# Performance work log

Hardware: AMD Instinct MI355X
Metric: run time of the kernel (lower is better)

Reference implementation:

```python
import jax, jax.numpy as jnp
import numpy as np

B, C, H, W = 8, 256, 128, 128
QK = 64

def setup_inputs() -> dict:
    key = jax.random.key(0)
    ks = jax.random.split(key, 8)
    s = 0.02
    return {
        "x": jax.random.normal(ks[0], (B, C, H, W), dtype=jnp.float32),
        "wq": jax.random.normal(ks[1], (QK, C), dtype=jnp.float32) * s,
        "bq": jax.random.normal(ks[2], (QK,), dtype=jnp.float32) * s,
        "wk": jax.random.normal(ks[3], (QK, C), dtype=jnp.float32) * s,
        "bk": jax.random.normal(ks[4], (QK,), dtype=jnp.float32) * s,
        "wv": jax.random.normal(ks[5], (C, C), dtype=jnp.float32) * s,
        "bv": jax.random.normal(ks[6], (C,), dtype=jnp.float32) * s,
        "gamma": jax.random.normal(ks[7], (1,), dtype=jnp.float32) * 0.1,
    }

def reference(x, wq, bq, wk, bk, wv, bv, gamma):
    # 1x1 convs == per-pixel linear projections over channels
    Q = jnp.einsum('bchw,oc->bohw', x, wq) + bq[None, :, None, None]  # (b,qk,h,w)
    K = jnp.einsum('bchw,oc->bohw', x, wk) + bk[None, :, None, None]  # (b,qk,h,w)
    V = jnp.einsum('bchw,oc->bohw', x, wv) + bv[None, :, None, None]  # (b,c,h,w)
    # row attention: for each (b,h) row, scores over width pairs
    scores = jnp.einsum('bchw,bchv->bhwv', Q, K)          # (b,h,w_q,w_k)
    attn = jax.nn.softmax(scores, axis=-1)                # softmax over keys (dim=2 after bmm)
    out = jnp.einsum('bchv,bhwv->bchw', V, attn)          # (b,c,h,w)
    return gamma[0] * out + x
```

## Files before the change

kernel.cpp:

```cpp
#include <hip/hip_runtime.h>
#include <hip/hip_bf16.h>


typedef short bf16x8 __attribute__((ext_vector_type(8)));
typedef float f32x4 __attribute__((ext_vector_type(4)));
using u32 = unsigned int;
using u16 = unsigned short;

#define XT_OFF   0
#define XT_SB    528
#define SA_OFF   67584
#define SB_OFF   85056
#define QT_OFF   67584
#define KT_OFF   86016
#define QK_SB    144
#define PL_OFF   67584
#define PL_SB    272
#define WP_OFF   104448
#define VL_OFF   141312
#define VL_SB    272
#define BIAS_OFF 158720
#define LDS_TOTAL 160256

#define WS_WQK   0
#define WS_WV    73728

__device__ __forceinline__ u16 bfbits(float f) {
    __hip_bfloat16 h = __float2bfloat16(f);
    u16 u; __builtin_memcpy(&u, &h, 2); return u;
}
__device__ __forceinline__ u32 packbf2(float a, float b) {
    return (u32)bfbits(a) | ((u32)bfbits(b) << 16);
}
__device__ __forceinline__ float bf2f(u16 u) {
    union { u32 i; float f; } v; v.i = ((u32)u) << 16; return v.f;
}

__device__ __forceinline__ void gl2lds16(const char* g, const char* l) {
    __builtin_amdgcn_global_load_lds(
        (const __attribute__((address_space(1))) void*)(unsigned long long)g,
        (__attribute__((address_space(3))) void*)(u32)(unsigned long long)l,
        16, 0, 0);
}
__device__ __forceinline__ void stage18k(const char* g, const char* lds, int w, int l) {
    gl2lds16(g + w * 1024 + l * 16,        lds + w * 1024);
    gl2lds16(g + 8192 + w * 1024 + l * 16, lds + 8192 + w * 1024);
    if (l < 16) gl2lds16(g + 16384 + w * 256 + l * 16, lds + 16384 + w * 256);
}
__device__ __forceinline__ void stage36k(const char* g, const char* lds, int w, int l) {
#pragma unroll
    for (int r = 0; r < 4; ++r)
        gl2lds16(g + r * 8192 + w * 1024 + l * 16, lds + r * 8192 + w * 1024);
    if (l < 32) gl2lds16(g + 32768 + w * 512 + l * 16, lds + 32768 + w * 512);
}

__device__ __forceinline__ void hard_barrier() {
    __builtin_amdgcn_sched_barrier(0);
    asm volatile("s_barrier" ::: "memory");
    __builtin_amdgcn_sched_barrier(0);
}

__global__ void prep_weights(const float* __restrict__ wq, const float* __restrict__ wk,
                             const float* __restrict__ wv, u32* __restrict__ ws) {
    int i = blockIdx.x * 256 + threadIdx.x;
    if (i >= 55296) return;
    u32 v = 0;
    if (i < 18432) {
        int c = i / 2304, rem = i % 2304;
        int row = rem / 36, iw = rem % 36;
        int kc = c >> 1;
        const float* m = (c & 1) ? wk : wq;
        if (iw < 32) {
            int col = kc * 64 + iw * 2;
            v = packbf2(m[row * 256 + col], m[row * 256 + col + 1]);
        }
    } else {
        int j = i - 18432;
        int c = j / 2304, rem = j % 2304;
        int row = rem / 36, iw = rem % 36;
        int mc = c >> 2, kc = c & 3;
        if (iw < 32) {
            int col = kc * 64 + iw * 2;
            v = packbf2(wv[(mc * 64 + row) * 256 + col], wv[(mc * 64 + row) * 256 + col + 1]);
        }
    }
    ws[i] = v;
}

__global__ __launch_bounds__(512, 1) void rowattn_mfma(
    const float* __restrict__ x,
    const float* __restrict__ bq,
    const float* __restrict__ bk,
    const float* __restrict__ bv,
    const float* __restrict__ gamma,
    const char* __restrict__ wsp,
    float* __restrict__ out)
{
    __shared__ __align__(16) char smem[LDS_TOTAL];
    const int t  = threadIdx.x;
    const int bh = blockIdx.x;
    const int b  = bh >> 7;
    const int h  = bh & 127;
    const int l  = t & 63;
    const int a  = l & 15;
    const int q  = l >> 4;
    const int nw = __builtin_amdgcn_readfirstlane(t >> 6);

    const char* wqk_g = wsp + WS_WQK;
    const char* wv_g  = wsp + WS_WV;
    const float g = gamma[0];

    stage18k(wqk_g,         smem + WP_OFF,         nw, l);
    stage18k(wqk_g + 18432, smem + WP_OFF + 18432, nw, l);

    float* biasl = (float*)(smem + BIAS_OFF);
    if (t < 384) {
        float v;
        if (t < 64) v = bq[t];
        else if (t < 128) v = bk[t - 64];
        else v = bv[t - 128];
        biasl[t] = v;
    }

    const int cl = t >> 5;
    const int w4 = (t & 31) * 4;
    const float* xb = x + ((b * 256 + cl) * 128 + h) * 128 + w4;
    float4 xr[16];
#pragma unroll
    for (int p = 0; p < 8; ++p) {
        xr[2 * p]     = *(const float4*)(xb + (p * 32) * 16384);
        xr[2 * p + 1] = *(const float4*)(xb + (p * 32 + 16) * 16384);
    }

    const int wrd = t >> 2;
    const int c8  = (t & 3) * 8;
#define SCW(c, w) ((c) * 136 + ((c) >> 3) * 8 + (w))
    {
        float* s0 = (float*)(smem + SA_OFF);
        *(float4*)&s0[SCW(cl, w4)]      = xr[0];
        *(float4*)&s0[SCW(cl + 16, w4)] = xr[1];
    }
    __syncthreads();
#pragma unroll
    for (int p = 0; p < 8; ++p) {
        float* sp = (float*)(smem + ((p & 1) ? SB_OFF : SA_OFF));
        if (p < 7) {
            float* sn = (float*)(smem + ((p & 1) ? SA_OFF : SB_OFF));
            *(float4*)&sn[SCW(cl, w4)]      = xr[2 * p + 2];
            *(float4*)&sn[SCW(cl + 16, w4)] = xr[2 * p + 3];
        }
        const float* sr = sp + SCW(c8, wrd);
        float s0 = sr[0],       s1 = sr[136],     s2 = sr[2 * 136], s3 = sr[3 * 136];
        float s4 = sr[4 * 136], s5 = sr[5 * 136], s6 = sr[6 * 136], s7 = sr[7 * 136];
        uint4 pk;
        pk.x = packbf2(s0, s1); pk.y = packbf2(s2, s3);
        pk.z = packbf2(s4, s5); pk.w = packbf2(s6, s7);
        *(uint4*)(smem + XT_OFF + wrd * XT_SB + (p * 32 + c8) * 2) = pk;
        __syncthreads();
    }
#undef SCW

    {
        f32x4 accQ[4], accK[4];
#pragma unroll
        for (int mt = 0; mt < 4; ++mt) {
            f32x4 cq, ck;
#pragma unroll
            for (int r = 0; r < 4; ++r) {
                cq[r] = biasl[mt * 16 + q * 4 + r];
                ck[r] = biasl[64 + mt * 16 + q * 4 + r];
            }
            accQ[mt] = cq; accK[mt] = ck;
        }
#pragma unroll
        for (int kc = 0; kc < 4; ++kc) {
            if (kc == 2) {
                asm volatile("s_waitcnt vmcnt(3)" ::: "memory");
                hard_barrier();
            }
            if (kc == 3) __syncthreads();
            const char* wqp = smem + WP_OFF + (kc & 1) * 18432;
            const char* wkp = wqp + 9216;
#pragma unroll
            for (int ks = 0; ks < 2; ++ks) {
                bf16x8 bx = *(const bf16x8*)(smem + XT_OFF + (nw * 16 + a) * XT_SB + (kc * 64 + ks * 32) * 2 + q * 16);
#pragma unroll
                for (int mt = 0; mt < 4; ++mt) {
                    bf16x8 aq = *(const bf16x8*)(wqp + (mt * 16 + a) * 144 + ks * 64 + q * 16);
                    accQ[mt] = __builtin_amdgcn_mfma_f32_16x16x32_bf16(aq, bx, accQ[mt], 0, 0, 0);
                    bf16x8 ak = *(const bf16x8*)(wkp + (mt * 16 + a) * 144 + ks * 64 + q * 16);
                    accK[mt] = __builtin_amdgcn_mfma_f32_16x16x32_bf16(ak, bx, accK[mt], 0, 0, 0);
                }
            }
            if (kc == 0) { __syncthreads(); stage18k(wqk_g + 2 * 18432, smem + WP_OFF,         nw, l); }
            if (kc == 1) { __syncthreads(); stage18k(wqk_g + 3 * 18432, smem + WP_OFF + 18432, nw, l); }
        }
#pragma unroll
        for (int mt = 0; mt < 4; ++mt) {
            uint2 pq; pq.x = packbf2(accQ[mt][0], accQ[mt][1]); pq.y = packbf2(accQ[mt][2], accQ[mt][3]);
            *(uint2*)(smem + QT_OFF + (nw * 16 + a) * QK_SB + (mt * 16 + q * 4) * 2) = pq;
            uint2 pk; pk.x = packbf2(accK[mt][0], accK[mt][1]); pk.y = packbf2(accK[mt][2], accK[mt][3]);
            *(uint2*)(smem + KT_OFF + (nw * 16 + a) * QK_SB + (mt * 16 + q * 4) * 2) = pk;
        }
    }
    __syncthreads();

    stage36k(wv_g, smem + WP_OFF, nw, l);
    f32x4 st[8];
#pragma unroll
    for (int mt = 0; mt < 8; ++mt) st[mt] = (f32x4){0.f, 0.f, 0.f, 0.f};
#pragma unroll
    for (int ks = 0; ks < 2; ++ks) {
        bf16x8 bqf = *(const bf16x8*)(smem + QT_OFF + (nw * 16 + a) * QK_SB + ks * 64 + q * 16);
#pragma unroll
        for (int mt = 0; mt < 8; ++mt) {
            bf16x8 akf = *(const bf16x8*)(smem + KT_OFF + (mt * 16 + a) * QK_SB + ks * 64 + q * 16);
            st[mt] = __builtin_amdgcn_mfma_f32_16x16x32_bf16(akf, bqf, st[mt], 0, 0, 0);
        }
    }
    {
        float mx = -3.0e38f;
#pragma unroll
        for (int mt = 0; mt < 8; ++mt)
#pragma unroll
            for (int r = 0; r < 4; ++r) mx = fmaxf(mx, st[mt][r]);
        mx = fmaxf(mx, __shfl_xor(mx, 16, 64));
        mx = fmaxf(mx, __shfl_xor(mx, 32, 64));
        float sum = 0.f;
#pragma unroll
        for (int mt = 0; mt < 8; ++mt)
#pragma unroll
            for (int r = 0; r < 4; ++r) { float e = __expf(st[mt][r] - mx); st[mt][r] = e; sum += e; }
        sum += __shfl_xor(sum, 16, 64);
        sum += __shfl_xor(sum, 32, 64);
        float inv = 1.0f / sum;
        hard_barrier();
#pragma unroll
        for (int mt = 0; mt < 8; ++mt) {
            uint2 pp; pp.x = packbf2(st[mt][0] * inv, st[mt][1] * inv);
            pp.y = packbf2(st[mt][2] * inv, st[mt][3] * inv);
            *(uint2*)(smem + PL_OFF + (nw * 16 + a) * PL_SB + (mt * 16 + q * 4) * 2) = pp;
        }
    }

#pragma unroll 1
    for (int mc = 0; mc < 4; ++mc) {
        __syncthreads();
        f32x4 accV[4];
#pragma unroll
        for (int mt = 0; mt < 4; ++mt) {
            f32x4 cv;
#pragma unroll
            for (int r = 0; r < 4; ++r) cv[r] = biasl[128 + mc * 64 + mt * 16 + q * 4 + r];
            accV[mt] = cv;
        }
#pragma unroll
        for (int kc = 0; kc < 4; ++kc) {
            const char* wvp = smem + WP_OFF + kc * 9216;
#pragma unroll
            for (int ks = 0; ks < 2; ++ks) {
                bf16x8 bx = *(const bf16x8*)(smem + XT_OFF + (nw * 16 + a) * XT_SB + (kc * 64 + ks * 32) * 2 + q * 16);
#pragma unroll
                for (int mt = 0; mt < 4; ++mt) {
                    bf16x8 av = *(const bf16x8*)(wvp + (mt * 16 + a) * 144 + ks * 64 + q * 16);
                    accV[mt] = __builtin_amdgcn_mfma_f32_16x16x32_bf16(av, bx, accV[mt], 0, 0, 0);
                }
            }
        }
#pragma unroll
        for (int mt = 0; mt < 4; ++mt)
#pragma unroll
            for (int r = 0; r < 4; ++r)
                *(u16*)(smem + VL_OFF + (mt * 16 + q * 4 + r) * VL_SB + (nw * 16 + a) * 2) = bfbits(accV[mt][r]);
        __syncthreads();
        if (mc < 3) stage36k(wv_g + (mc + 1) * 36864, smem + WP_OFF, nw, l);
        f32x4 accO[4];
#pragma unroll
        for (int mt = 0; mt < 4; ++mt) accO[mt] = (f32x4){0.f, 0.f, 0.f, 0.f};
#pragma unroll
        for (int ks = 0; ks < 4; ++ks) {
            bf16x8 bp = *(const bf16x8*)(smem + PL_OFF + (nw * 16 + a) * PL_SB + ks * 64 + q * 16);
#pragma unroll
            for (int mt = 0; mt < 4; ++mt) {
                bf16x8 av = *(const bf16x8*)(smem + VL_OFF + (mt * 16 + a) * VL_SB + ks * 64 + q * 16);
                accO[mt] = __builtin_amdgcn_mfma_f32_16x16x32_bf16(av, bp, accO[mt], 0, 0, 0);
            }
        }
#pragma unroll
        for (int mt = 0; mt < 4; ++mt) {
#pragma unroll
            for (int r = 0; r < 4; ++r) {
                int c = mc * 64 + mt * 16 + q * 4 + r;
                int w = nw * 16 + a;
                u16 xv = *(const u16*)(smem + XT_OFF + w * XT_SB + c * 2);
                out[((b * 256 + c) * 128 + h) * 128 + w] = g * accO[mt][r] + bf2f(xv);
            }
        }
    }
}

extern "C" void kernel_launch(void* const* d_in, const int* in_sizes, int n_in,
                              void* d_out, int out_size, void* d_ws, size_t ws_size,
                              hipStream_t stream) {
    const float* x     = (const float*)d_in[0];
    const float* wq    = (const float*)d_in[1];
    const float* bq    = (const float*)d_in[2];
    const float* wk    = (const float*)d_in[3];
    const float* bk    = (const float*)d_in[4];
    const float* wv    = (const float*)d_in[5];
    const float* bv    = (const float*)d_in[6];
    const float* gamma = (const float*)d_in[7];
    float* out = (float*)d_out;

    hipLaunchKernelGGL(prep_weights, dim3(216), dim3(256), 0, stream, wq, wk, wv, (u32*)d_ws);
    hipLaunchKernelGGL(rowattn_mfma, dim3(1024), dim3(512), 0, stream,
                       x, bq, bk, bv, gamma, (const char*)d_ws, out);
}
```

Before: 338.4 us.

## Double workgroup to 16 waves with 2D wave tiling and split-softmax merge

Raises the block from 8 to 16 waves and tiles each GEMM stage over a 4x4 wave grid (output-row tile by 32-wide pixel tile) instead of giving each wave a 16-pixel strip. Softmax across keys is now split over four waves, with per-wave max and sum merged through LDS. The aim is more waves to hide latency and fewer registers per thread (fewer x loads held, smaller accumulators). The cost is extra barriers and an LDS reduction step for the softmax. Operand reuse per wave also drops, so more LDS fragment loads are issued per MFMA.

```diff
diff --git a/kernel.cpp b/kernel.cpp
--- a/kernel.cpp
+++ b/kernel.cpp
@@ -19,6 +19,7 @@
 #define WP_OFF   104448
 #define VL_OFF   141312
 #define VL_SB    272
+#define SMP_OFF  141312
 #define BIAS_OFF 158720
 #define LDS_TOTAL 160256
 
@@ -43,20 +44,23 @@
         16, 0, 0);
 }
 __device__ __forceinline__ void stage18k(const char* g, const char* lds, int w, int l) {
-    gl2lds16(g + w * 1024 + l * 16,        lds + w * 1024);
-    gl2lds16(g + 8192 + w * 1024 + l * 16, lds + 8192 + w * 1024);
-    if (l < 16) gl2lds16(g + 16384 + w * 256 + l * 16, lds + 16384 + w * 256);
+    gl2lds16(g + w * 1024 + l * 16, lds + w * 1024);
+    if (l < 8) gl2lds16(g + 16384 + w * 128 + l * 16, lds + 16384 + w * 128);
 }
 __device__ __forceinline__ void stage36k(const char* g, const char* lds, int w, int l) {
-#pragma unroll
-    for (int r = 0; r < 4; ++r)
-        gl2lds16(g + r * 8192 + w * 1024 + l * 16, lds + r * 8192 + w * 1024);
-    if (l < 32) gl2lds16(g + 32768 + w * 512 + l * 16, lds + 32768 + w * 512);
+    gl2lds16(g + w * 1024 + l * 16,         lds + w * 1024);
+    gl2lds16(g + 16384 + w * 1024 + l * 16, lds + 16384 + w * 1024);
+    if (l < 16) gl2lds16(g + 32768 + w * 256 + l * 16, lds + 32768 + w * 256);
 }
 
 __device__ __forceinline__ void hard_barrier() {
     __builtin_amdgcn_sched_barrier(0);
     asm volatile("s_barrier" ::: "memory");
+    __builtin_amdgcn_sched_barrier(0);
+}
+__device__ __forceinline__ void lgkm_barrier() {
+    __builtin_amdgcn_sched_barrier(0);
+    asm volatile("s_waitcnt lgkmcnt(0)\n\ts_barrier" ::: "memory");
     __builtin_amdgcn_sched_barrier(0);
 }
 
@@ -87,7 +91,7 @@
     ws[i] = v;
 }
 
-__global__ __launch_bounds__(512, 1) void rowattn_mfma(
+__global__ __launch_bounds__(1024, 1) void rowattn_mfma(
     const float* __restrict__ x,
     const float* __restrict__ bq,
     const float* __restrict__ bk,
@@ -104,14 +108,17 @@
     const int l  = t & 63;
     const int a  = l & 15;
     const int q  = l >> 4;
-    const int nw = __builtin_amdgcn_readfirstlane(t >> 6);
+    const int wid = __builtin_amdgcn_readfirstlane(t >> 6);
+    const int mi = wid >> 2;
+    const int nj = wid & 3;
+    const int w0 = nj * 32;
 
     const char* wqk_g = wsp + WS_WQK;
     const char* wv_g  = wsp + WS_WV;
     const float g = gamma[0];
 
-    stage18k(wqk_g,         smem + WP_OFF,         nw, l);
-    stage18k(wqk_g + 18432, smem + WP_OFF + 18432, nw, l);
+    stage18k(wqk_g,         smem + WP_OFF,         wid, l);
+    stage18k(wqk_g + 18432, smem + WP_OFF + 18432, wid, l);
 
     float* biasl = (float*)(smem + BIAS_OFF);
     if (t < 384) {
@@ -125,57 +132,50 @@
     const int cl = t >> 5;
     const int w4 = (t & 31) * 4;
     const float* xb = x + ((b * 256 + cl) * 128 + h) * 128 + w4;
-    float4 xr[16];
-#pragma unroll
-    for (int p = 0; p < 8; ++p) {
-        xr[2 * p]     = *(const float4*)(xb + (p * 32) * 16384);
-        xr[2 * p + 1] = *(const float4*)(xb + (p * 32 + 16) * 16384);
-    }
-
-    const int wrd = t >> 2;
-    const int c8  = (t & 3) * 8;
+    float4 xr[8];
+#pragma unroll
+    for (int p = 0; p < 8; ++p) xr[p] = *(const float4*)(xb + (p * 32) * 16384);
+
+    const int wrd = t >> 3;
+    const int c4  = (t & 7) * 4;
 #define SCW(c, w) ((c) * 136 + ((c) >> 3) * 8 + (w))
     {
         float* s0 = (float*)(smem + SA_OFF);
-        *(float4*)&s0[SCW(cl, w4)]      = xr[0];
-        *(float4*)&s0[SCW(cl + 16, w4)] = xr[1];
-    }
-    __syncthreads();
+        *(float4*)&s0[SCW(cl, w4)] = xr[0];
+    }
+    lgkm_barrier();
 #pragma unroll
     for (int p = 0; p < 8; ++p) {
         float* sp = (float*)(smem + ((p & 1) ? SB_OFF : SA_OFF));
         if (p < 7) {
             float* sn = (float*)(smem + ((p & 1) ? SA_OFF : SB_OFF));
-            *(float4*)&sn[SCW(cl, w4)]      = xr[2 * p + 2];
-            *(float4*)&sn[SCW(cl + 16, w4)] = xr[2 * p + 3];
-        }
-        const float* sr = sp + SCW(c8, wrd);
-        float s0 = sr[0],       s1 = sr[136],     s2 = sr[2 * 136], s3 = sr[3 * 136];
-        float s4 = sr[4 * 136], s5 = sr[5 * 136], s6 = sr[6 * 136], s7 = sr[7 * 136];
-        uint4 pk;
-        pk.x = packbf2(s0, s1); pk.y = packbf2(s2, s3);
-        pk.z = packbf2(s4, s5); pk.w = packbf2(s6, s7);
-        *(uint4*)(smem + XT_OFF + wrd * XT_SB + (p * 32 + c8) * 2) = pk;
-        __syncthreads();
+            *(float4*)&sn[SCW(cl, w4)] = xr[p + 1];
+        }
+        const float* sr = sp + SCW(c4, wrd);
+        float s0 = sr[0], s1 = sr[136], s2 = sr[2 * 136], s3 = sr[3 * 136];
+        uint2 pk; pk.x = packbf2(s0, s1); pk.y = packbf2(s2, s3);
+        *(uint2*)(smem + XT_OFF + wrd * XT_SB + (p * 32 + c4) * 2) = pk;
+        if (p < 7) lgkm_barrier();
     }
 #undef SCW
+    __syncthreads();
 
     {
-        f32x4 accQ[4], accK[4];
-#pragma unroll
-        for (int mt = 0; mt < 4; ++mt) {
+        f32x4 accQ[2], accK[2];
+#pragma unroll
+        for (int nt = 0; nt < 2; ++nt) {
             f32x4 cq, ck;
 #pragma unroll
             for (int r = 0; r < 4; ++r) {
-                cq[r] = biasl[mt * 16 + q * 4 + r];
-                ck[r] = biasl[64 + mt * 16 + q * 4 + r];
-            }
-            accQ[mt] = cq; accK[mt] = ck;
+                cq[r] = biasl[mi * 16 + q * 4 + r];
+                ck[r] = biasl[64 + mi * 16 + q * 4 + r];
+            }
+            accQ[nt] = cq; accK[nt] = ck;
         }
 #pragma unroll
         for (int kc = 0; kc < 4; ++kc) {
             if (kc == 2) {
-                asm volatile("s_waitcnt vmcnt(3)" ::: "memory");
+                asm volatile("s_waitcnt vmcnt(2)" ::: "memory");
                 hard_barrier();
             }
             if (kc == 3) __syncthreads();
@@ -183,117 +183,150 @@
             const char* wkp = wqp + 9216;
 #pragma unroll
             for (int ks = 0; ks < 2; ++ks) {
-                bf16x8 bx = *(const bf16x8*)(smem + XT_OFF + (nw * 16 + a) * XT_SB + (kc * 64 + ks * 32) * 2 + q * 16);
-#pragma unroll
-                for (int mt = 0; mt < 4; ++mt) {
-                    bf16x8 aq = *(const bf16x8*)(wqp + (mt * 16 + a) * 144 + ks * 64 + q * 16);
-                    accQ[mt] = __builtin_amdgcn_mfma_f32_16x16x32_bf16(aq, bx, accQ[mt], 0, 0, 0);
-                    bf16x8 ak = *(const bf16x8*)(wkp + (mt * 16 + a) * 144 + ks * 64 + q * 16);
-                    accK[mt] = __builtin_amdgcn_mfma_f32_16x16x32_bf16(ak, bx, accK[mt], 0, 0, 0);
+                bf16x8 aq = *(const bf16x8*)(wqp + (mi * 16 + a) * 144 + ks * 64 + q * 16);
+                bf16x8 ak = *(const bf16x8*)(wkp + (mi * 16 + a) * 144 + ks * 64 + q * 16);
+#pragma unroll
+                for (int nt = 0; nt < 2; ++nt) {
+                    bf16x8 bx = *(const bf16x8*)(smem + XT_OFF + (w0 + nt * 16 + a) * XT_SB + (kc * 64 + ks * 32) * 2 + q * 16);
+                    accQ[nt] = __builtin_amdgcn_mfma_f32_16x16x32_bf16(aq, bx, accQ[nt], 0, 0, 0);
+                    accK[nt] = __builtin_amdgcn_mfma_f32_16x16x32_bf16(ak, bx, accK[nt], 0, 0, 0);
                 }
             }
-            if (kc == 0) { __syncthreads(); stage18k(wqk_g + 2 * 18432, smem + WP_OFF,         nw, l); }
-            if (kc == 1) { __syncthreads(); stage18k(wqk_g + 3 * 18432, smem + WP_OFF + 18432, nw, l); }
-        }
-#pragma unroll
-        for (int mt = 0; mt < 4; ++mt) {
-            uint2 pq; pq.x = packbf2(accQ[mt][0], accQ[mt][1]); pq.y = packbf2(accQ[mt][2], accQ[mt][3]);
-            *(uint2*)(smem + QT_OFF + (nw * 16 + a) * QK_SB + (mt * 16 + q * 4) * 2) = pq;
-            uint2 pk; pk.x = packbf2(accK[mt][0], accK[mt][1]); pk.y = packbf2(accK[mt][2], accK[mt][3]);
-            *(uint2*)(smem + KT_OFF + (nw * 16 + a) * QK_SB + (mt * 16 + q * 4) * 2) = pk;
+            if (kc == 0) { hard_barrier(); stage18k(wqk_g + 2 * 18432, smem + WP_OFF,         wid, l); }
+            if (kc == 1) { hard_barrier(); stage18k(wqk_g + 3 * 18432, smem + WP_OFF + 18432, wid, l); }
+        }
+#pragma unroll
+        for (int nt = 0; nt < 2; ++nt) {
+            const int wrow = w0 + nt * 16 + a;
+            uint2 pq; pq.x = packbf2(accQ[nt][0], accQ[nt][1]); pq.y = packbf2(accQ[nt][2], accQ[nt][3]);
+            *(uint2*)(smem + QT_OFF + wrow * QK_SB + (mi * 16 + q * 4) * 2) = pq;
+            uint2 pk; pk.x = packbf2(accK[nt][0], accK[nt][1]); pk.y = packbf2(accK[nt][2], accK[nt][3]);
+            *(uint2*)(smem + KT_OFF + wrow * QK_SB + (mi * 16 + q * 4) * 2) = pk;
         }
     }
     __syncthreads();
 
-    stage36k(wv_g, smem + WP_OFF, nw, l);
-    f32x4 st[8];
-#pragma unroll
-    for (int mt = 0; mt < 8; ++mt) st[mt] = (f32x4){0.f, 0.f, 0.f, 0.f};
+    stage36k(wv_g, smem + WP_OFF, wid, l);
+    f32x4 st[2][2];
+#pragma unroll
+    for (int mt2 = 0; mt2 < 2; ++mt2)
+#pragma unroll
+        for (int nt = 0; nt < 2; ++nt) st[mt2][nt] = (f32x4){0.f, 0.f, 0.f, 0.f};
 #pragma unroll
     for (int ks = 0; ks < 2; ++ks) {
-        bf16x8 bqf = *(const bf16x8*)(smem + QT_OFF + (nw * 16 + a) * QK_SB + ks * 64 + q * 16);
-#pragma unroll
-        for (int mt = 0; mt < 8; ++mt) {
-            bf16x8 akf = *(const bf16x8*)(smem + KT_OFF + (mt * 16 + a) * QK_SB + ks * 64 + q * 16);
-            st[mt] = __builtin_amdgcn_mfma_f32_16x16x32_bf16(akf, bqf, st[mt], 0, 0, 0);
-        }
+        bf16x8 bq0 = *(const bf16x8*)(smem + QT_OFF + (w0 + a) * QK_SB + ks * 64 + q * 16);
+        bf16x8 bq1 = *(const bf16x8*)(smem + QT_OFF + (w0 + 16 + a) * QK_SB + ks * 64 + q * 16);
+        bf16x8 ak0 = *(const bf16x8*)(smem + KT_OFF + (mi * 32 + a) * QK_SB + ks * 64 + q * 16);
+        bf16x8 ak1 = *(const bf16x8*)(smem + KT_OFF + (mi * 32 + 16 + a) * QK_SB + ks * 64 + q * 16);
+        st[0][0] = __builtin_amdgcn_mfma_f32_16x16x32_bf16(ak0, bq0, st[0][0], 0, 0, 0);
+        st[0][1] = __builtin_amdgcn_mfma_f32_16x16x32_bf16(ak0, bq1, st[0][1], 0, 0, 0);
+        st[1][0] = __builtin_amdgcn_mfma_f32_16x16x32_bf16(ak1, bq0, st[1][0], 0, 0, 0);
+        st[1][1] = __builtin_amdgcn_mfma_f32_16x16x32_bf16(ak1, bq1, st[1][1], 0, 0, 0);
     }
     {
-        float mx = -3.0e38f;
-#pragma unroll
-        for (int mt = 0; mt < 8; ++mt)
-#pragma unroll
-            for (int r = 0; r < 4; ++r) mx = fmaxf(mx, st[mt][r]);
-        mx = fmaxf(mx, __shfl_xor(mx, 16, 64));
-        mx = fmaxf(mx, __shfl_xor(mx, 32, 64));
-        float sum = 0.f;
-#pragma unroll
-        for (int mt = 0; mt < 8; ++mt)
-#pragma unroll
-            for (int r = 0; r < 4; ++r) { float e = __expf(st[mt][r] - mx); st[mt][r] = e; sum += e; }
-        sum += __shfl_xor(sum, 16, 64);
-        sum += __shfl_xor(sum, 32, 64);
-        float inv = 1.0f / sum;
-        hard_barrier();
-#pragma unroll
-        for (int mt = 0; mt < 8; ++mt) {
-            uint2 pp; pp.x = packbf2(st[mt][0] * inv, st[mt][1] * inv);
-            pp.y = packbf2(st[mt][2] * inv, st[mt][3] * inv);
-            *(uint2*)(smem + PL_OFF + (nw * 16 + a) * PL_SB + (mt * 16 + q * 4) * 2) = pp;
+        float pmax[2], psum[2];
+#pragma unroll
+        for (int nt = 0; nt < 2; ++nt) {
+            float mx = -3.0e38f;
+#pragma unroll
+            for (int mt2 = 0; mt2 < 2; ++mt2)
+#pragma unroll
+                for (int r = 0; r < 4; ++r) mx = fmaxf(mx, st[mt2][nt][r]);
+            mx = fmaxf(mx, __shfl_xor(mx, 16, 64));
+            mx = fmaxf(mx, __shfl_xor(mx, 32, 64));
+            float s = 0.f;
+#pragma unroll
+            for (int mt2 = 0; mt2 < 2; ++mt2)
+#pragma unroll
+                for (int r = 0; r < 4; ++r) {
+                    float e = __expf(st[mt2][nt][r] - mx); st[mt2][nt][r] = e; s += e;
+                }
+            s += __shfl_xor(s, 16, 64);
+            s += __shfl_xor(s, 32, 64);
+            pmax[nt] = mx; psum[nt] = s;
+        }
+        float2* smp = (float2*)(smem + SMP_OFF);
+        if (q == 0) {
+#pragma unroll
+            for (int nt = 0; nt < 2; ++nt)
+                smp[(w0 + nt * 16 + a) * 4 + mi] = make_float2(pmax[nt], psum[nt]);
+        }
+        lgkm_barrier();
+        float f[2];
+#pragma unroll
+        for (int nt = 0; nt < 2; ++nt) {
+            const int wq = w0 + nt * 16 + a;
+            float2 p0 = smp[wq * 4 + 0], p1 = smp[wq * 4 + 1];
+            float2 p2 = smp[wq * 4 + 2], p3 = smp[wq * 4 + 3];
+            float m = fmaxf(fmaxf(p0.x, p1.x), fmaxf(p2.x, p3.x));
+            float s = p0.y * __expf(p0.x - m) + p1.y * __expf(p1.x - m)
+                    + p2.y * __expf(p2.x - m) + p3.y * __expf(p3.x - m);
+            f[nt] = __expf(pmax[nt] - m) / s;
+        }
+#pragma unroll
+        for (int nt = 0; nt < 2; ++nt) {
+            const int wq = w0 + nt * 16 + a;
+#pragma unroll
+            for (int mt2 = 0; mt2 < 2; ++mt2) {
+                uint2 pp;
+                pp.x = packbf2(st[mt2][nt][0] * f[nt], st[mt2][nt][1] * f[nt]);
+                pp.y = packbf2(st[mt2][nt][2] * f[nt], st[mt2][nt][3] * f[nt]);
+                *(uint2*)(smem + PL_OFF + wq * PL_SB + (mi * 32 + mt2 * 16 + q * 4) * 2) = pp;
+            }
         }
     }
 
 #pragma unroll 1
     for (int mc = 0; mc < 4; ++mc) {
         __syncthreads();
-        f32x4 accV[4];
-#pragma unroll
-        for (int mt = 0; mt < 4; ++mt) {
+        f32x4 accV[2];
+        {
             f32x4 cv;
 #pragma unroll
-            for (int r = 0; r < 4; ++r) cv[r] = biasl[128 + mc * 64 + mt * 16 + q * 4 + r];
-            accV[mt] = cv;
+            for (int r = 0; r < 4; ++r) cv[r] = biasl[128 + mc * 64 + mi * 16 + q * 4 + r];
+            accV[0] = cv; accV[1] = cv;
         }
 #pragma unroll
         for (int kc = 0; kc < 4; ++kc) {
             const char* wvp = smem + WP_OFF + kc * 9216;
 #pragma unroll
             for (int ks = 0; ks < 2; ++ks) {
-                bf16x8 bx = *(const bf16x8*)(smem + XT_OFF + (nw * 16 + a) * XT_SB + (kc * 64 + ks * 32) * 2 + q * 16);
-#pragma unroll
-                for (int mt = 0; mt < 4; ++mt) {
-                    bf16x8 av = *(const bf16x8*)(wvp + (mt * 16 + a) * 144 + ks * 64 + q * 16);
-                    accV[mt] = __builtin_amdgcn_mfma_f32_16x16x32_bf16(av, bx, accV[mt], 0, 0, 0);
+                bf16x8 av = *(const bf16x8*)(wvp + (mi * 16 + a) * 144 + ks * 64 + q * 16);
+#pragma unroll
+                for (int nt = 0; nt < 2; ++nt) {
+                    bf16x8 bx = *(const bf16x8*)(smem + XT_OFF + (w0 + nt * 16 + a) * XT_SB + (kc * 64 + ks * 32) * 2 + q * 16);
+                    accV[nt] = __builtin_amdgcn_mfma_f32_16x16x32_bf16(av, bx, accV[nt], 0, 0, 0);
                 }
             }
         }
 #pragma unroll
-        for (int mt = 0; mt < 4; ++mt)
+        for (int nt = 0; nt < 2; ++nt)
 #pragma unroll
             for (int r = 0; r < 4; ++r)
-                *(u16*)(smem + VL_OFF + (mt * 16 + q * 4 + r) * VL_SB + (nw * 16 + a) * 2) = bfbits(accV[mt][r]);
+                *(u16*)(smem + VL_OFF + (mi * 16 + q * 4 + r) * VL_SB + (w0 + nt * 16 + a) * 2) = bfbits(accV[nt][r]);
         __syncthreads();
-        if (mc < 3) stage36k(wv_g + (mc + 1) * 36864, smem + WP_OFF, nw, l);
-        f32x4 accO[4];
-#pragma unroll
-        for (int mt = 0; mt < 4; ++mt) accO[mt] = (f32x4){0.f, 0.f, 0.f, 0.f};
+        if (mc < 3) stage36k(wv_g + (mc + 1) * 36864, smem + WP_OFF, wid, l);
+        f32x4 accO[2];
+        accO[0] = (f32x4){0.f, 0.f, 0.f, 0.f};
+        accO[1] = (f32x4){0.f, 0.f, 0.f, 0.f};
 #pragma unroll
         for (int ks = 0; ks < 4; ++ks) {
-            bf16x8 bp = *(const bf16x8*)(smem + PL_OFF + (nw * 16 + a) * PL_SB + ks * 64 + q * 16);
-#pragma unroll
-            for (int mt = 0; mt < 4; ++mt) {
-                bf16x8 av = *(const bf16x8*)(smem + VL_OFF + (mt * 16 + a) * VL_SB + ks * 64 + q * 16);
-                accO[mt] = __builtin_amdgcn_mfma_f32_16x16x32_bf16(av, bp, accO[mt], 0, 0, 0);
-            }
-        }
-#pragma unroll
-        for (int mt = 0; mt < 4; ++mt) {
-#pragma unroll
-            for (int r = 0; r < 4; ++r) {
-                int c = mc * 64 + mt * 16 + q * 4 + r;
-                int w = nw * 16 + a;
+            bf16x8 av = *(const bf16x8*)(smem + VL_OFF + (mi * 16 + a) * VL_SB + ks * 64 + q * 16);
+#pragma unroll
+            for (int nt = 0; nt < 2; ++nt) {
+                bf16x8 bp = *(const bf16x8*)(smem + PL_OFF + (w0 + nt * 16 + a) * PL_SB + ks * 64 + q * 16);
+                accO[nt] = __builtin_amdgcn_mfma_f32_16x16x32_bf16(av, bp, accO[nt], 0, 0, 0);
+            }
+        }
+#pragma unroll
+        for (int r = 0; r < 4; ++r) {
+            const int c = mc * 64 + mi * 16 + q * 4 + r;
+            float* orow = out + ((b * 256 + c) * 128 + h) * 128;
+#pragma unroll
+            for (int nt = 0; nt < 2; ++nt) {
+                const int w = w0 + nt * 16 + a;
                 u16 xv = *(const u16*)(smem + XT_OFF + w * XT_SB + c * 2);
-                out[((b * 256 + c) * 128 + h) * 128 + w] = g * accO[mt][r] + bf2f(xv);
+                orow[w] = g * accO[nt][r] + bf2f(xv);
             }
         }
     }
@@ -313,6 +346,6 @@
     float* out = (float*)d_out;
 
     hipLaunchKernelGGL(prep_weights, dim3(216), dim3(256), 0, stream, wq, wk, wv, (u32*)d_ws);
-    hipLaunchKernelGGL(rowattn_mfma, dim3(1024), dim3(512), 0, stream,
+    hipLaunchKernelGGL(rowattn_mfma, dim3(1024), dim3(1024), 0, stream,
                        x, bq, bk, bv, gamma, (const char*)d_ws, out);
 }
```

Measured after the change: 295.5 us. 1.14x faster.
